# Kernel optimization log

Measured on AMD Instinct MI355X. Metric: run time of the kernel, lower is better.

Reference implementation:

```python
import jax, jax.numpy as jnp
import numpy as np

EMBED_DIM = 1280
NUM_HEADS = 20
HEAD_DIM = EMBED_DIM // NUM_HEADS


def setup_inputs() -> dict:
    key = jax.random.key(0)
    ks = jax.random.split(key, 9)
    s = 0.02
    return {
        "hidden_states": jax.random.normal(ks[0], (4, 1500, EMBED_DIM), dtype=jnp.float32),
        "q_w": jax.random.normal(ks[1], (EMBED_DIM, EMBED_DIM), dtype=jnp.float32) * s,
        "q_b": jax.random.normal(ks[2], (EMBED_DIM,), dtype=jnp.float32) * s,
        "k_w": jax.random.normal(ks[3], (EMBED_DIM, EMBED_DIM), dtype=jnp.float32) * s,
        "v_w": jax.random.normal(ks[4], (EMBED_DIM, EMBED_DIM), dtype=jnp.float32) * s,
        "v_b": jax.random.normal(ks[5], (EMBED_DIM,), dtype=jnp.float32) * s,
        "o_w": jax.random.normal(ks[6], (EMBED_DIM, EMBED_DIM), dtype=jnp.float32) * s,
        "o_b": jax.random.normal(ks[7], (EMBED_DIM,), dtype=jnp.float32) * s,
    }


def reference(hidden_states, q_w, q_b, k_w, v_w, v_b, o_w, o_b):
    B, T, E = hidden_states.shape
    H, D = NUM_HEADS, HEAD_DIM
    scaling = D ** (-0.5)
    # projections (torch Linear: x @ W^T + b)
    q = (hidden_states @ q_w.T + q_b) * scaling
    k = hidden_states @ k_w.T  # k_proj has bias=False
    v = hidden_states @ v_w.T + v_b
    # [B, H, T, D]
    q = q.reshape(B, T, H, D).transpose(0, 2, 1, 3)
    k = k.reshape(B, T, H, D).transpose(0, 2, 1, 3)
    v = v.reshape(B, T, H, D).transpose(0, 2, 1, 3)
    # NOTE: module divides by sqrt(head_dim) AGAIN inside the kernel (faithful)
    scores = jnp.einsum("bhqd,bhkd->bhqk", q, k) / jnp.sqrt(jnp.asarray(D, q.dtype))
    attn = jax.nn.softmax(scores, axis=-1)
    out = jnp.einsum("bhqk,bhkd->bhqd", attn, v)
    out = out.transpose(0, 2, 1, 3).reshape(B, T, E)
    return out @ o_w.T + o_b
```

## Files before the change

kernel.cpp:

```cpp
#include <hip/hip_runtime.h>

typedef __attribute__((ext_vector_type(4))) float f32x4;
typedef __attribute__((ext_vector_type(8))) __bf16 bf16x8;
typedef __attribute__((ext_vector_type(4))) __bf16 bf16x4;

#define DEV __device__ __forceinline__

DEV f32x4 mfma_bf16(bf16x8 a, bf16x8 b, f32x4 c) {
  return __builtin_amdgcn_mfma_f32_16x16x32_bf16(a, b, c, 0, 0, 0);
}

DEV void glds16(const void* gp, void* lp) {
  __builtin_amdgcn_global_load_lds((const __attribute__((address_space(1))) void*)gp,
                                   (__attribute__((address_space(3))) void*)lp, 16, 0, 0);
}

DEV float fast_exp2(float x) {
#if __has_builtin(__builtin_amdgcn_exp2f)
  return __builtin_amdgcn_exp2f(x);
#else
  float r;
  asm("v_exp_f32 %0, %1" : "=v"(r) : "v"(x));
  return r;
#endif
}

#define SB0() __builtin_amdgcn_sched_barrier(0)

__global__ __launch_bounds__(256) void cvt_all(const float* __restrict__ hs,
                                               const float* __restrict__ qw,
                                               const float* __restrict__ kw,
                                               const float* __restrict__ vw,
                                               const float* __restrict__ ow,
                                               __bf16* __restrict__ oX,
                                               __bf16* __restrict__ oQ,
                                               __bf16* __restrict__ oK,
                                               __bf16* __restrict__ oV,
                                               __bf16* __restrict__ oO) {
  const int blk = blockIdx.x;
  if (blk < 3840) {
    long long e = ((long long)blk * 256 + threadIdx.x) * 8;
    bf16x8 o = {};
    if (e < 7680000) {
      const f32x4* ip = (const f32x4*)(hs + e);
      f32x4 a = ip[0], b = ip[1];
#pragma unroll
      for (int j = 0; j < 4; ++j) { o[j] = (__bf16)a[j]; o[j + 4] = (__bf16)b[j]; }
    }
    *(bf16x8*)(oX + e) = o;
  } else {
    const int wb = blk - 3840;
    const int which = wb / 800;
    const int bb = wb - which * 800;
    const float* in = which == 0 ? qw : which == 1 ? kw : which == 2 ? vw : ow;
    __bf16* out = which == 0 ? oQ : which == 1 ? oK : which == 2 ? oV : oO;
    long long e = ((long long)bb * 256 + threadIdx.x) * 8;
    const f32x4* ip = (const f32x4*)(in + e);
    f32x4 x = ip[0], y = ip[1];
    bf16x8 o;
#pragma unroll
    for (int j = 0; j < 4; ++j) { o[j] = (__bf16)x[j]; o[j + 4] = (__bf16)y[j]; }
    *(bf16x8*)(out + e) = o;
  }
}

__global__ __launch_bounds__(512, 2) void gemm_qkv(const __bf16* __restrict__ A,
                                                   const __bf16* __restrict__ Bw,
                                                   const float* __restrict__ qbias,
                                                   const float* __restrict__ vbias,
                                                   __bf16* __restrict__ Qo,
                                                   __bf16* __restrict__ Ko,
                                                   __bf16* __restrict__ Vto,
                                                   float sq) {
  __shared__ __align__(16) __bf16 lds[3 * 24576];
  const int tid = threadIdx.x;
  const int lane = tid & 63, wave = tid >> 6;
  const int wrow = wave >> 2, wcol = wave & 3;
  const int r = lane & 15, g = lane >> 4;

  const int orig = blockIdx.x;
  const int xcd = orig & 7, ii = orig >> 3;
  const int m_idx = xcd * 6 + ii % 6;
  const int n_idx = ii / 6;
  const int m0 = m_idx * 128, n0 = n_idx * 256;

  const f32x4 fz = {0.f, 0.f, 0.f, 0.f};
  f32x4 acc[4][4];
#pragma unroll
  for (int mi = 0; mi < 4; ++mi)
#pragma unroll
    for (int ni = 0; ni < 4; ++ni) acc[mi][ni] = fz;

  const __bf16* srcA[2];
  const __bf16* srcB[4];
#pragma unroll
  for (int j = 0; j < 2; ++j) {
    const int slot = j * 512 + tid;
    const int row = slot >> 3, ch = slot & 7;
    srcA[j] = A + (size_t)(m0 + row) * 1280 + (ch ^ (row & 7)) * 8;
  }
#pragma unroll
  for (int j = 0; j < 4; ++j) {
    const int slot = j * 512 + tid;
    const int row = slot >> 3, ch = slot & 7;
    srcB[j] = Bw + (size_t)(n0 + row) * 1280 + (ch ^ (row & 7)) * 8;
  }
  const int wdst = wave * 512;

  auto stage_h0 = [&](int buf, int kt2) {
    const int k0 = kt2 * 64;
    glds16(srcA[0] + k0, &lds[buf * 24576 + wdst]);
    glds16(srcA[1] + k0, &lds[buf * 24576 + 4096 + wdst]);
    glds16(srcB[0] + k0, &lds[buf * 24576 + 8192 + wdst]);
  };
  auto stage_h1 = [&](int buf, int kt2) {
    const int k0 = kt2 * 64;
    glds16(srcB[1] + k0, &lds[buf * 24576 + 12288 + wdst]);
    glds16(srcB[2] + k0, &lds[buf * 24576 + 16384 + wdst]);
    glds16(srcB[3] + k0, &lds[buf * 24576 + 20480 + wdst]);
  };

  stage_h0(0, 0); stage_h1(0, 0);
  stage_h0(1, 1); stage_h1(1, 1);
  asm volatile("s_waitcnt vmcnt(6)" ::: "memory");
  SB0();
  __builtin_amdgcn_s_barrier();
  SB0();

  const int aoff = (wrow * 64 + r) * 64;
  const int boff = 8192 + (wcol * 64 + r) * 64;
  const int c0 = (g ^ (r & 7)) * 8;
  const int c1 = ((4 + g) ^ (r & 7)) * 8;

  int cur = 0;
  for (int kt = 0; kt < 20; ++kt) {
    int nxt2 = cur + 2; if (nxt2 >= 3) nxt2 -= 3;
    const __bf16* Lb = &lds[cur * 24576];
    const bool pf = (kt + 2 < 20);

    bf16x8 af[4], bfr[4];
#pragma unroll
    for (int mi = 0; mi < 4; ++mi) af[mi] = *(const bf16x8*)&Lb[aoff + mi * 1024 + c0];
#pragma unroll
    for (int ni = 0; ni < 4; ++ni) bfr[ni] = *(const bf16x8*)&Lb[boff + ni * 1024 + c0];
    if (pf) stage_h0(nxt2, kt + 2);
    asm volatile("s_waitcnt lgkmcnt(0)" ::: "memory");
    SB0();
    __builtin_amdgcn_s_setprio(1);
#pragma unroll
    for (int mi = 0; mi < 4; ++mi)
#pragma unroll
      for (int ni = 0; ni < 4; ++ni)
        acc[mi][ni] = mfma_bf16(af[mi], bfr[ni], acc[mi][ni]);
    __builtin_amdgcn_s_setprio(0);

    bf16x8 af1[4], bfr1[4];
#pragma unroll
    for (int mi = 0; mi < 4; ++mi) af1[mi] = *(const bf16x8*)&Lb[aoff + mi * 1024 + c1];
#pragma unroll
    for (int ni = 0; ni < 4; ++ni) bfr1[ni] = *(const bf16x8*)&Lb[boff + ni * 1024 + c1];
    if (pf) stage_h1(nxt2, kt + 2);
    asm volatile("s_waitcnt lgkmcnt(0)" ::: "memory");
    SB0();
    __builtin_amdgcn_s_setprio(1);
#pragma unroll
    for (int mi = 0; mi < 4; ++mi)
#pragma unroll
      for (int ni = 0; ni < 4; ++ni)
        acc[mi][ni] = mfma_bf16(af1[mi], bfr1[ni], acc[mi][ni]);
    __builtin_amdgcn_s_setprio(0);

    if (pf) asm volatile("s_waitcnt vmcnt(6)" ::: "memory");
    else    asm volatile("s_waitcnt vmcnt(0)" ::: "memory");
    SB0();
    __builtin_amdgcn_s_barrier();
    SB0();
    cur = cur + 1; if (cur >= 3) cur -= 3;
  }

  const int which = n_idx / 5;
  const int nb = n0 - which * 1280 + wcol * 64;
  const float scale = (which == 0) ? sq : 1.f;

#pragma unroll
  for (int ni = 0; ni < 4; ++ni) {
    const int col = nb + ni * 16 + r;
    const float bv = (which == 0) ? qbias[col] : (which == 2) ? vbias[col] : 0.f;
#pragma unroll
    for (int mi = 0; mi < 4; ++mi) {
      if (which == 2) {
        const int row0 = m0 + wrow * 64 + mi * 16 + g * 4;
        if (row0 < 6000) {
          const int bidx = row0 / 1500;
          const int t = row0 - bidx * 1500;
          union { __bf16 h[4]; unsigned long long u; } pk;
#pragma unroll
          for (int rr = 0; rr < 4; ++rr) pk.h[rr] = (__bf16)(acc[mi][ni][rr] + bv);
          *(unsigned long long*)&Vto[((size_t)(bidx * 1280 + col)) * 1536 + t] = pk.u;
        }
      } else {
        __bf16* dst = (which == 0) ? Qo : Ko;
#pragma unroll
        for (int rr = 0; rr < 4; ++rr) {
          const int row = m0 + wrow * 64 + mi * 16 + g * 4 + rr;
          dst[(size_t)row * 1280 + col] = (__bf16)((acc[mi][ni][rr] + bv) * scale);
        }
      }
    }
  }
}

__global__ __launch_bounds__(512, 2) void gemm_o(const __bf16* __restrict__ A,
                                                 const __bf16* __restrict__ Bw,
                                                 const float* __restrict__ bias,
                                                 float* __restrict__ out) {
  __shared__ __align__(16) __bf16 lds[3 * 24576];
  const int tid = threadIdx.x;
  const int lane = tid & 63, wave = tid >> 6;
  const int wrow = wave >> 2, wcol = wave & 3;
  const int r = lane & 15, g = lane >> 4;

  const int orig = blockIdx.x;
  const int xcd = orig & 7, ii = orig >> 3;
  const int m_idx = xcd * 6 + ii % 6;
  const int n_idx = ii / 6;
  const int m0 = m_idx * 128, n0 = n_idx * 256;

  const f32x4 fz = {0.f, 0.f, 0.f, 0.f};
  f32x4 acc[4][4];
#pragma unroll
  for (int mi = 0; mi < 4; ++mi)
#pragma unroll
    for (int ni = 0; ni < 4; ++ni) acc[mi][ni] = fz;

  const __bf16* srcA[2];
  const __bf16* srcB[4];
#pragma unroll
  for (int j = 0; j < 2; ++j) {
    const int slot = j * 512 + tid;
    const int row = slot >> 3, ch = slot & 7;
    srcA[j] = A + (size_t)(m0 + row) * 1280 + (ch ^ (row & 7)) * 8;
  }
#pragma unroll
  for (int j = 0; j < 4; ++j) {
    const int slot = j * 512 + tid;
    const int row = slot >> 3, ch = slot & 7;
    srcB[j] = Bw + (size_t)(n0 + row) * 1280 + (ch ^ (row & 7)) * 8;
  }
  const int wdst = wave * 512;

  auto stage_h0 = [&](int buf, int kt2) {
    const int k0 = kt2 * 64;
    glds16(srcA[0] + k0, &lds[buf * 24576 + wdst]);
    glds16(srcA[1] + k0, &lds[buf * 24576 + 4096 + wdst]);
    glds16(srcB[0] + k0, &lds[buf * 24576 + 8192 + wdst]);
  };
  auto stage_h1 = [&](int buf, int kt2) {
    const int k0 = kt2 * 64;
    glds16(srcB[1] + k0, &lds[buf * 24576 + 12288 + wdst]);
    glds16(srcB[2] + k0, &lds[buf * 24576 + 16384 + wdst]);
    glds16(srcB[3] + k0, &lds[buf * 24576 + 20480 + wdst]);
  };

  stage_h0(0, 0); stage_h1(0, 0);
  stage_h0(1, 1); stage_h1(1, 1);
  asm volatile("s_waitcnt vmcnt(6)" ::: "memory");
  SB0();
  __builtin_amdgcn_s_barrier();
  SB0();

  const int aoff = (wrow * 64 + r) * 64;
  const int boff = 8192 + (wcol * 64 + r) * 64;
  const int c0 = (g ^ (r & 7)) * 8;
  const int c1 = ((4 + g) ^ (r & 7)) * 8;

  int cur = 0;
  for (int kt = 0; kt < 20; ++kt) {
    int nxt2 = cur + 2; if (nxt2 >= 3) nxt2 -= 3;
    const __bf16* Lb = &lds[cur * 24576];
    const bool pf = (kt + 2 < 20);

    bf16x8 af[4], bfr[4];
#pragma unroll
    for (int mi = 0; mi < 4; ++mi) af[mi] = *(const bf16x8*)&Lb[aoff + mi * 1024 + c0];
#pragma unroll
    for (int ni = 0; ni < 4; ++ni) bfr[ni] = *(const bf16x8*)&Lb[boff + ni * 1024 + c0];
    if (pf) stage_h0(nxt2, kt + 2);
    asm volatile("s_waitcnt lgkmcnt(0)" ::: "memory");
    SB0();
    __builtin_amdgcn_s_setprio(1);
#pragma unroll
    for (int mi = 0; mi < 4; ++mi)
#pragma unroll
      for (int ni = 0; ni < 4; ++ni)
        acc[mi][ni] = mfma_bf16(af[mi], bfr[ni], acc[mi][ni]);
    __builtin_amdgcn_s_setprio(0);

    bf16x8 af1[4], bfr1[4];
#pragma unroll
    for (int mi = 0; mi < 4; ++mi) af1[mi] = *(const bf16x8*)&Lb[aoff + mi * 1024 + c1];
#pragma unroll
    for (int ni = 0; ni < 4; ++ni) bfr1[ni] = *(const bf16x8*)&Lb[boff + ni * 1024 + c1];
    if (pf) stage_h1(nxt2, kt + 2);
    asm volatile("s_waitcnt lgkmcnt(0)" ::: "memory");
    SB0();
    __builtin_amdgcn_s_setprio(1);
#pragma unroll
    for (int mi = 0; mi < 4; ++mi)
#pragma unroll
      for (int ni = 0; ni < 4; ++ni)
        acc[mi][ni] = mfma_bf16(af1[mi], bfr1[ni], acc[mi][ni]);
    __builtin_amdgcn_s_setprio(0);

    if (pf) asm volatile("s_waitcnt vmcnt(6)" ::: "memory");
    else    asm volatile("s_waitcnt vmcnt(0)" ::: "memory");
    SB0();
    __builtin_amdgcn_s_barrier();
    SB0();
    cur = cur + 1; if (cur >= 3) cur -= 3;
  }

#pragma unroll
  for (int ni = 0; ni < 4; ++ni) {
    const int col = n0 + wcol * 64 + ni * 16 + r;
    const float bv = bias[col];
#pragma unroll
    for (int mi = 0; mi < 4; ++mi) {
#pragma unroll
      for (int rr = 0; rr < 4; ++rr) {
        const int row = m0 + wrow * 64 + mi * 16 + g * 4 + rr;
        if (row < 6000) out[(size_t)row * 1280 + col] = acc[mi][ni][rr] + bv;
      }
    }
  }
}

__global__ __launch_bounds__(256) void flash_attn(const __bf16* __restrict__ Qg,
                                                  const __bf16* __restrict__ Kg,
                                                  const __bf16* __restrict__ Vt,
                                                  __bf16* __restrict__ Og) {
  constexpr int TQ = 1500, NKT = 24;
  __shared__ __align__(16) __bf16 lds[16384];

  const int tid = threadIdx.x;
  const int lane = tid & 63, w = tid >> 6;
  const int r = lane & 15, g = lane >> 4;

  const int orig = blockIdx.x;
  const int work = (orig & 7) * 120 + (orig >> 3);
  const int bh = work / 12, qb = work - bh * 12;
  const int b = bh / 20, h = bh - b * 20;
  const int q0 = qb * 128;
  const size_t base = (size_t)b * (TQ * 1280) + h * 64;
  const __bf16* Vt_bh = Vt + (size_t)(b * 1280 + h * 64) * 1536;

  const int k_src_col = 8 * ((lane & 7) ^ (lane >> 3));
  const int k_row_loc = w * 8 + (lane >> 3);
  const int v_d_loc = 8 * w + (lane >> 3);
  const int v_chunk = 8 * ((lane & 7) ^ (lane >> 3));

  bf16x8 qf[2][2];
#pragma unroll
  for (int qs = 0; qs < 2; ++qs) {
    int t = q0 + w * 32 + qs * 16 + r;
    t = t < TQ ? t : TQ - 1;
    const __bf16* qp = Qg + base + (size_t)t * 1280;
#pragma unroll
    for (int dk = 0; dk < 2; ++dk) qf[qs][dk] = *(const bf16x8*)(qp + dk * 32 + g * 8);
  }

  const f32x4 fz = {0.f, 0.f, 0.f, 0.f};
  f32x4 o_acc[2][4];
#pragma unroll
  for (int qs = 0; qs < 2; ++qs)
#pragma unroll
    for (int ni = 0; ni < 4; ++ni) o_acc[qs][ni] = fz;
  float l_run[2] = {0.f, 0.f};

  auto stage = [&](int buf, int kt2) {
    const int kb = kt2 * 64;
#pragma unroll
    for (int i = 0; i < 2; ++i) {
      int row = kb + i * 32 + k_row_loc;
      row = row < TQ ? row : TQ - 1;
      glds16(Kg + base + (size_t)row * 1280 + k_src_col,
             &lds[buf * 8192 + i * 2048 + w * 512]);
    }
#pragma unroll
    for (int i = 0; i < 2; ++i) {
      glds16(Vt_bh + (size_t)(32 * i + v_d_loc) * 1536 + kb + v_chunk,
             &lds[buf * 8192 + 4096 + i * 2048 + w * 512]);
    }
  };

  stage(0, 0);
  for (int kt = 0; kt < NKT; ++kt) {
    const int cur = kt & 1;
    if (kt + 1 < NKT) {
      stage(cur ^ 1, kt + 1);
      asm volatile("s_waitcnt vmcnt(4)" ::: "memory");
    } else {
      asm volatile("s_waitcnt vmcnt(0)" ::: "memory");
    }
    SB0();
    __builtin_amdgcn_s_barrier();
    SB0();

    const __bf16* Kb = &lds[cur * 8192];

    f32x4 s[2][4];
#pragma unroll
    for (int qs = 0; qs < 2; ++qs)
#pragma unroll
      for (int nt = 0; nt < 4; ++nt) s[qs][nt] = fz;
#pragma unroll
    for (int dk = 0; dk < 2; ++dk) {
      bf16x8 kf[4];
#pragma unroll
      for (int nt = 0; nt < 4; ++nt) {
        const int row = nt * 16 + r;
        const int sc = (dk * 32 + g * 8) ^ ((r & 7) << 3);
        kf[nt] = *(const bf16x8*)&Kb[row * 64 + sc];
      }
#pragma unroll
      for (int qs = 0; qs < 2; ++qs)
#pragma unroll
        for (int nt = 0; nt < 4; ++nt) s[qs][nt] = mfma_bf16(kf[nt], qf[qs][dk], s[qs][nt]);
    }

    if (kt == NKT - 1) {
#pragma unroll
      for (int nt = 0; nt < 4; ++nt)
#pragma unroll
        for (int rr = 0; rr < 4; ++rr) {
          const int key = kt * 64 + nt * 16 + g * 4 + rr;
          if (key >= TQ) { s[0][nt][rr] = -1.0e30f; s[1][nt][rr] = -1.0e30f; }
        }
    }

#pragma unroll
    for (int qs = 0; qs < 2; ++qs) {
      float ssum = 0.f;
#pragma unroll
      for (int nt = 0; nt < 4; ++nt)
#pragma unroll
        for (int rr = 0; rr < 4; ++rr) {
          const float p = fast_exp2(s[qs][nt][rr]);
          s[qs][nt][rr] = p;
          ssum += p;
        }
      l_run[qs] += ssum;
    }

    const __bf16* Vbuf = &lds[cur * 8192 + 4096];
    const int swz = (r & 7) << 3;
#pragma unroll
    for (int ks = 0; ks < 2; ++ks) {
      bf16x8 pa[2];
#pragma unroll
      for (int qs = 0; qs < 2; ++qs) {
        bf16x8 t;
#pragma unroll
        for (int j = 0; j < 4; ++j) {
          t[j] = (__bf16)s[qs][2 * ks][j];
          t[4 + j] = (__bf16)s[qs][2 * ks + 1][j];
        }
        pa[qs] = t;
      }
      const int o1 = (32 * ks + 4 * g) ^ swz;
      const int o2 = (32 * ks + 16 + 4 * g) ^ swz;
#pragma unroll
      for (int ni = 0; ni < 4; ++ni) {
        const int dbase = (16 * ni + r) * 64;
        union { bf16x4 hh[2]; bf16x8 v; } u;
        u.hh[0] = *(const bf16x4*)&Vbuf[dbase + o1];
        u.hh[1] = *(const bf16x4*)&Vbuf[dbase + o2];
#pragma unroll
        for (int qs = 0; qs < 2; ++qs) o_acc[qs][ni] = mfma_bf16(u.v, pa[qs], o_acc[qs][ni]);
      }
    }

    asm volatile("s_waitcnt lgkmcnt(0)" ::: "memory");
    SB0();
    __builtin_amdgcn_s_barrier();
    SB0();
  }

  float inv[2];
#pragma unroll
  for (int qs = 0; qs < 2; ++qs) {
    float l = l_run[qs];
    l += __shfl_xor(l, 16);
    l += __shfl_xor(l, 32);
    inv[qs] = 1.0f / l;
  }

  __bf16* Ob = &lds[w * 2304];
#pragma unroll
  for (int qs = 0; qs < 2; ++qs) {
#pragma unroll
    for (int ni = 0; ni < 4; ++ni)
#pragma unroll
      for (int rr = 0; rr < 4; ++rr)
        Ob[(qs * 16 + r) * 72 + ni * 16 + g * 4 + rr] = (__bf16)(o_acc[qs][ni][rr] * inv[qs]);
  }
  __syncthreads();
  const int qg = q0 + w * 32 + (lane >> 1);
  if (qg < TQ) {
#pragma unroll
    for (int v = 0; v < 4; ++v) {
      const int c = (lane & 1) * 32 + v * 8;
      bf16x8 val = *(const bf16x8*)&lds[w * 2304 + (lane >> 1) * 72 + c];
      *(bf16x8*)&Og[base + (size_t)qg * 1280 + c] = val;
    }
  }
}

extern "C" void kernel_launch(void* const* d_in, const int* in_sizes, int n_in,
                              void* d_out, int out_size, void* d_ws, size_t ws_size,
                              hipStream_t stream) {
  const float* hs = (const float*)d_in[0];
  const float* qw = (const float*)d_in[1];
  const float* qb = (const float*)d_in[2];
  const float* kw = (const float*)d_in[3];
  const float* vw = (const float*)d_in[4];
  const float* vb = (const float*)d_in[5];
  const float* ow = (const float*)d_in[6];
  const float* ob = (const float*)d_in[7];

  const long long MP = 6144LL * 1280;
  const long long WE = 1280LL * 1280;
  __bf16* Xb = (__bf16*)d_ws;
  __bf16* Wq = Xb + MP;
  __bf16* Wk = Wq + WE;
  __bf16* Wv = Wk + WE;
  __bf16* Wo = Wv + WE;
  __bf16* Qb = Wo + WE;
  __bf16* Kb = Qb + MP;
  __bf16* Vtb = Kb + MP;
  __bf16* Ab = Xb;

  cvt_all<<<7040, 256, 0, stream>>>(hs, qw, kw, vw, ow, Xb, Wq, Wk, Wv, Wo);

  const float SQ = 1.4426950408889634f / 64.f;
  gemm_qkv<<<720, 512, 0, stream>>>(Xb, Wq, qb, vb, Qb, Kb, Vtb, SQ);

  flash_attn<<<960, 256, 0, stream>>>(Qb, Kb, Vtb, Ab);

  gemm_o<<<240, 512, 0, stream>>>(Ab, Wo, ob, (float*)d_out);
}
```

Baseline: 175.7 us.

## Load K and V fragments directly from global memory into registers in flash attention

```diff
diff --git a/kernel.cpp b/kernel.cpp
--- a/kernel.cpp
+++ b/kernel.cpp
@@ -340,7 +340,7 @@
                                                   const __bf16* __restrict__ Vt,
                                                   __bf16* __restrict__ Og) {
   constexpr int TQ = 1500, NKT = 24;
-  __shared__ __align__(16) __bf16 lds[16384];
+  __shared__ __align__(16) __bf16 lds[4 * 2304];
 
   const int tid = threadIdx.x;
   const int lane = tid & 63, w = tid >> 6;
@@ -354,11 +354,6 @@
   const size_t base = (size_t)b * (TQ * 1280) + h * 64;
   const __bf16* Vt_bh = Vt + (size_t)(b * 1280 + h * 64) * 1536;
 
-  const int k_src_col = 8 * ((lane & 7) ^ (lane >> 3));
-  const int k_row_loc = w * 8 + (lane >> 3);
-  const int v_d_loc = 8 * w + (lane >> 3);
-  const int v_chunk = 8 * ((lane & 7) ^ (lane >> 3));
-
   bf16x8 qf[2][2];
 #pragma unroll
   for (int qs = 0; qs < 2; ++qs) {
@@ -377,36 +372,33 @@
     for (int ni = 0; ni < 4; ++ni) o_acc[qs][ni] = fz;
   float l_run[2] = {0.f, 0.f};
 
-  auto stage = [&](int buf, int kt2) {
-    const int kb = kt2 * 64;
-#pragma unroll
-    for (int i = 0; i < 2; ++i) {
-      int row = kb + i * 32 + k_row_loc;
+  const __bf16* vrow[4];
+#pragma unroll
+  for (int ni = 0; ni < 4; ++ni) vrow[ni] = Vt_bh + (size_t)(16 * ni + r) * 1536 + 4 * g;
+
+  for (int kt = 0; kt < NKT; ++kt) {
+    const int kb = kt * 64;
+
+    bf16x8 kf[2][4];
+#pragma unroll
+    for (int nt = 0; nt < 4; ++nt) {
+      int row = kb + nt * 16 + r;
       row = row < TQ ? row : TQ - 1;
-      glds16(Kg + base + (size_t)row * 1280 + k_src_col,
-             &lds[buf * 8192 + i * 2048 + w * 512]);
-    }
-#pragma unroll
-    for (int i = 0; i < 2; ++i) {
-      glds16(Vt_bh + (size_t)(32 * i + v_d_loc) * 1536 + kb + v_chunk,
-             &lds[buf * 8192 + 4096 + i * 2048 + w * 512]);
-    }
-  };
-
-  stage(0, 0);
-  for (int kt = 0; kt < NKT; ++kt) {
-    const int cur = kt & 1;
-    if (kt + 1 < NKT) {
-      stage(cur ^ 1, kt + 1);
-      asm volatile("s_waitcnt vmcnt(4)" ::: "memory");
-    } else {
-      asm volatile("s_waitcnt vmcnt(0)" ::: "memory");
-    }
-    SB0();
-    __builtin_amdgcn_s_barrier();
-    SB0();
-
-    const __bf16* Kb = &lds[cur * 8192];
+      const __bf16* kp = Kg + base + (size_t)row * 1280 + g * 8;
+      kf[0][nt] = *(const bf16x8*)kp;
+      kf[1][nt] = *(const bf16x8*)(kp + 32);
+    }
+
+    bf16x4 vfl[2][4][2];
+#pragma unroll
+    for (int ni = 0; ni < 4; ++ni) {
+      const __bf16* vp = vrow[ni] + kb;
+#pragma unroll
+      for (int ks = 0; ks < 2; ++ks) {
+        vfl[ks][ni][0] = *(const bf16x4*)(vp + 32 * ks);
+        vfl[ks][ni][1] = *(const bf16x4*)(vp + 32 * ks + 16);
+      }
+    }
 
     f32x4 s[2][4];
 #pragma unroll
@@ -414,26 +406,19 @@
 #pragma unroll
       for (int nt = 0; nt < 4; ++nt) s[qs][nt] = fz;
 #pragma unroll
-    for (int dk = 0; dk < 2; ++dk) {
-      bf16x8 kf[4];
-#pragma unroll
-      for (int nt = 0; nt < 4; ++nt) {
-        const int row = nt * 16 + r;
-        const int sc = (dk * 32 + g * 8) ^ ((r & 7) << 3);
-        kf[nt] = *(const bf16x8*)&Kb[row * 64 + sc];
-      }
+    for (int dk = 0; dk < 2; ++dk)
 #pragma unroll
       for (int qs = 0; qs < 2; ++qs)
 #pragma unroll
-        for (int nt = 0; nt < 4; ++nt) s[qs][nt] = mfma_bf16(kf[nt], qf[qs][dk], s[qs][nt]);
-    }
+        for (int nt = 0; nt < 4; ++nt)
+          s[qs][nt] = mfma_bf16(kf[dk][nt], qf[qs][dk], s[qs][nt]);
 
     if (kt == NKT - 1) {
 #pragma unroll
       for (int nt = 0; nt < 4; ++nt)
 #pragma unroll
         for (int rr = 0; rr < 4; ++rr) {
-          const int key = kt * 64 + nt * 16 + g * 4 + rr;
+          const int key = kb + nt * 16 + g * 4 + rr;
           if (key >= TQ) { s[0][nt][rr] = -1.0e30f; s[1][nt][rr] = -1.0e30f; }
         }
     }
@@ -452,8 +437,6 @@
       l_run[qs] += ssum;
     }
 
-    const __bf16* Vbuf = &lds[cur * 8192 + 4096];
-    const int swz = (r & 7) << 3;
 #pragma unroll
     for (int ks = 0; ks < 2; ++ks) {
       bf16x8 pa[2];
@@ -467,23 +450,15 @@
         }
         pa[qs] = t;
       }
-      const int o1 = (32 * ks + 4 * g) ^ swz;
-      const int o2 = (32 * ks + 16 + 4 * g) ^ swz;
 #pragma unroll
       for (int ni = 0; ni < 4; ++ni) {
-        const int dbase = (16 * ni + r) * 64;
         union { bf16x4 hh[2]; bf16x8 v; } u;
-        u.hh[0] = *(const bf16x4*)&Vbuf[dbase + o1];
-        u.hh[1] = *(const bf16x4*)&Vbuf[dbase + o2];
+        u.hh[0] = vfl[ks][ni][0];
+        u.hh[1] = vfl[ks][ni][1];
 #pragma unroll
         for (int qs = 0; qs < 2; ++qs) o_acc[qs][ni] = mfma_bf16(u.v, pa[qs], o_acc[qs][ni]);
       }
     }
-
-    asm volatile("s_waitcnt lgkmcnt(0)" ::: "memory");
-    SB0();
-    __builtin_amdgcn_s_barrier();
-    SB0();
   }
 
   float inv[2];
```

Result: slower. 419.6 us (+138.8%).

## Split flash attention across eight waves of sixteen queries each

Applied to the files above, without the earlier changes.

```diff
diff --git a/kernel.cpp b/kernel.cpp
--- a/kernel.cpp
+++ b/kernel.cpp
@@ -335,7 +335,7 @@
   }
 }
 
-__global__ __launch_bounds__(256) void flash_attn(const __bf16* __restrict__ Qg,
+__global__ __launch_bounds__(512) void flash_attn(const __bf16* __restrict__ Qg,
                                                   const __bf16* __restrict__ Kg,
                                                   const __bf16* __restrict__ Vt,
                                                   __bf16* __restrict__ Og) {
@@ -354,65 +354,45 @@
   const size_t base = (size_t)b * (TQ * 1280) + h * 64;
   const __bf16* Vt_bh = Vt + (size_t)(b * 1280 + h * 64) * 1536;
 
-  const int k_src_col = 8 * ((lane & 7) ^ (lane >> 3));
   const int k_row_loc = w * 8 + (lane >> 3);
-  const int v_d_loc = 8 * w + (lane >> 3);
-  const int v_chunk = 8 * ((lane & 7) ^ (lane >> 3));
-
-  bf16x8 qf[2][2];
-#pragma unroll
-  for (int qs = 0; qs < 2; ++qs) {
-    int t = q0 + w * 32 + qs * 16 + r;
+  const int kv_chunk = 8 * ((lane & 7) ^ (lane >> 3));
+
+  bf16x8 qf[2];
+  {
+    int t = q0 + w * 16 + r;
     t = t < TQ ? t : TQ - 1;
     const __bf16* qp = Qg + base + (size_t)t * 1280;
 #pragma unroll
-    for (int dk = 0; dk < 2; ++dk) qf[qs][dk] = *(const bf16x8*)(qp + dk * 32 + g * 8);
+    for (int dk = 0; dk < 2; ++dk) qf[dk] = *(const bf16x8*)(qp + dk * 32 + g * 8);
   }
 
   const f32x4 fz = {0.f, 0.f, 0.f, 0.f};
-  f32x4 o_acc[2][4];
-#pragma unroll
-  for (int qs = 0; qs < 2; ++qs)
-#pragma unroll
-    for (int ni = 0; ni < 4; ++ni) o_acc[qs][ni] = fz;
-  float l_run[2] = {0.f, 0.f};
+  f32x4 o_acc[4];
+#pragma unroll
+  for (int ni = 0; ni < 4; ++ni) o_acc[ni] = fz;
+  float l_run = 0.f;
 
   auto stage = [&](int buf, int kt2) {
     const int kb = kt2 * 64;
-#pragma unroll
-    for (int i = 0; i < 2; ++i) {
-      int row = kb + i * 32 + k_row_loc;
-      row = row < TQ ? row : TQ - 1;
-      glds16(Kg + base + (size_t)row * 1280 + k_src_col,
-             &lds[buf * 8192 + i * 2048 + w * 512]);
-    }
-#pragma unroll
-    for (int i = 0; i < 2; ++i) {
-      glds16(Vt_bh + (size_t)(32 * i + v_d_loc) * 1536 + kb + v_chunk,
-             &lds[buf * 8192 + 4096 + i * 2048 + w * 512]);
-    }
+    int row = kb + k_row_loc;
+    row = row < TQ ? row : TQ - 1;
+    glds16(Kg + base + (size_t)row * 1280 + kv_chunk,
+           &lds[buf * 8192 + w * 512]);
+    glds16(Vt_bh + (size_t)k_row_loc * 1536 + kb + kv_chunk,
+           &lds[buf * 8192 + 4096 + w * 512]);
   };
 
   stage(0, 0);
+  __syncthreads();
   for (int kt = 0; kt < NKT; ++kt) {
     const int cur = kt & 1;
-    if (kt + 1 < NKT) {
-      stage(cur ^ 1, kt + 1);
-      asm volatile("s_waitcnt vmcnt(4)" ::: "memory");
-    } else {
-      asm volatile("s_waitcnt vmcnt(0)" ::: "memory");
-    }
-    SB0();
-    __builtin_amdgcn_s_barrier();
-    SB0();
+    if (kt + 1 < NKT) stage(cur ^ 1, kt + 1);
 
     const __bf16* Kb = &lds[cur * 8192];
 
-    f32x4 s[2][4];
-#pragma unroll
-    for (int qs = 0; qs < 2; ++qs)
-#pragma unroll
-      for (int nt = 0; nt < 4; ++nt) s[qs][nt] = fz;
+    f32x4 s[4];
+#pragma unroll
+    for (int nt = 0; nt < 4; ++nt) s[nt] = fz;
 #pragma unroll
     for (int dk = 0; dk < 2; ++dk) {
       bf16x8 kf[4];
@@ -423,9 +403,7 @@
         kf[nt] = *(const bf16x8*)&Kb[row * 64 + sc];
       }
 #pragma unroll
-      for (int qs = 0; qs < 2; ++qs)
-#pragma unroll
-        for (int nt = 0; nt < 4; ++nt) s[qs][nt] = mfma_bf16(kf[nt], qf[qs][dk], s[qs][nt]);
+      for (int nt = 0; nt < 4; ++nt) s[nt] = mfma_bf16(kf[nt], qf[dk], s[nt]);
     }
 
     if (kt == NKT - 1) {
@@ -434,38 +412,32 @@
 #pragma unroll
         for (int rr = 0; rr < 4; ++rr) {
           const int key = kt * 64 + nt * 16 + g * 4 + rr;
-          if (key >= TQ) { s[0][nt][rr] = -1.0e30f; s[1][nt][rr] = -1.0e30f; }
+          if (key >= TQ) s[nt][rr] = -1.0e30f;
         }
     }
 
-#pragma unroll
-    for (int qs = 0; qs < 2; ++qs) {
+    {
       float ssum = 0.f;
 #pragma unroll
       for (int nt = 0; nt < 4; ++nt)
 #pragma unroll
         for (int rr = 0; rr < 4; ++rr) {
-          const float p = fast_exp2(s[qs][nt][rr]);
-          s[qs][nt][rr] = p;
+          const float p = fast_exp2(s[nt][rr]);
+          s[nt][rr] = p;
           ssum += p;
         }
-      l_run[qs] += ssum;
+      l_run += ssum;
     }
 
     const __bf16* Vbuf = &lds[cur * 8192 + 4096];
     const int swz = (r & 7) << 3;
 #pragma unroll
     for (int ks = 0; ks < 2; ++ks) {
-      bf16x8 pa[2];
-#pragma unroll
-      for (int qs = 0; qs < 2; ++qs) {
-        bf16x8 t;
-#pragma unroll
-        for (int j = 0; j < 4; ++j) {
-          t[j] = (__bf16)s[qs][2 * ks][j];
-          t[4 + j] = (__bf16)s[qs][2 * ks + 1][j];
-        }
-        pa[qs] = t;
+      bf16x8 pa;
+#pragma unroll
+      for (int j = 0; j < 4; ++j) {
+        pa[j] = (__bf16)s[2 * ks][j];
+        pa[4 + j] = (__bf16)s[2 * ks + 1][j];
       }
       const int o1 = (32 * ks + 4 * g) ^ swz;
       const int o2 = (32 * ks + 16 + 4 * g) ^ swz;
@@ -475,42 +447,31 @@
         union { bf16x4 hh[2]; bf16x8 v; } u;
         u.hh[0] = *(const bf16x4*)&Vbuf[dbase + o1];
         u.hh[1] = *(const bf16x4*)&Vbuf[dbase + o2];
-#pragma unroll
-        for (int qs = 0; qs < 2; ++qs) o_acc[qs][ni] = mfma_bf16(u.v, pa[qs], o_acc[qs][ni]);
+        o_acc[ni] = mfma_bf16(u.v, pa, o_acc[ni]);
       }
     }
 
-    asm volatile("s_waitcnt lgkmcnt(0)" ::: "memory");
-    SB0();
-    __builtin_amdgcn_s_barrier();
-    SB0();
-  }
-
-  float inv[2];
-#pragma unroll
-  for (int qs = 0; qs < 2; ++qs) {
-    float l = l_run[qs];
-    l += __shfl_xor(l, 16);
-    l += __shfl_xor(l, 32);
-    inv[qs] = 1.0f / l;
-  }
-
-  __bf16* Ob = &lds[w * 2304];
-#pragma unroll
-  for (int qs = 0; qs < 2; ++qs) {
-#pragma unroll
-    for (int ni = 0; ni < 4; ++ni)
-#pragma unroll
-      for (int rr = 0; rr < 4; ++rr)
-        Ob[(qs * 16 + r) * 72 + ni * 16 + g * 4 + rr] = (__bf16)(o_acc[qs][ni][rr] * inv[qs]);
-  }
+    __syncthreads();
+  }
+
+  float l = l_run;
+  l += __shfl_xor(l, 16);
+  l += __shfl_xor(l, 32);
+  const float inv = 1.0f / l;
+
+  __bf16* Ob = &lds[w * 1152];
+#pragma unroll
+  for (int ni = 0; ni < 4; ++ni)
+#pragma unroll
+    for (int rr = 0; rr < 4; ++rr)
+      Ob[r * 72 + ni * 16 + g * 4 + rr] = (__bf16)(o_acc[ni][rr] * inv);
   __syncthreads();
-  const int qg = q0 + w * 32 + (lane >> 1);
+  const int qg = q0 + w * 16 + (lane >> 2);
   if (qg < TQ) {
 #pragma unroll
-    for (int v = 0; v < 4; ++v) {
-      const int c = (lane & 1) * 32 + v * 8;
-      bf16x8 val = *(const bf16x8*)&lds[w * 2304 + (lane >> 1) * 72 + c];
+    for (int v = 0; v < 2; ++v) {
+      const int c = (lane & 3) * 16 + v * 8;
+      bf16x8 val = *(const bf16x8*)&lds[w * 1152 + (lane >> 2) * 72 + c];
       *(bf16x8*)&Og[base + (size_t)qg * 1280 + c] = val;
     }
   }
@@ -545,7 +506,7 @@
   const float SQ = 1.4426950408889634f / 64.f;
   gemm_qkv<<<720, 512, 0, stream>>>(Xb, Wq, qb, vb, Qb, Kb, Vtb, SQ);
 
-  flash_attn<<<960, 256, 0, stream>>>(Qb, Kb, Vtb, Ab);
+  flash_attn<<<960, 512, 0, stream>>>(Qb, Kb, Vtb, Ab);
 
   gemm_o<<<240, 512, 0, stream>>>(Ab, Wo, ob, (float*)d_out);
 }
```

After: 175.4 us. Within noise of the previous version (-0.2%).

## Compute softmax row sums with MFMA, merge barriers, prioritize MFMA waves

Applied to the files above, without the earlier changes.

```diff
diff --git a/kernel.cpp b/kernel.cpp
--- a/kernel.cpp
+++ b/kernel.cpp
@@ -369,13 +369,18 @@
     for (int dk = 0; dk < 2; ++dk) qf[qs][dk] = *(const bf16x8*)(qp + dk * 32 + g * 8);
   }
 
+  bf16x8 ones;
+#pragma unroll
+  for (int j = 0; j < 8; ++j) ones[j] = (__bf16)1.0f;
+
   const f32x4 fz = {0.f, 0.f, 0.f, 0.f};
-  f32x4 o_acc[2][4];
-#pragma unroll
-  for (int qs = 0; qs < 2; ++qs)
+  f32x4 o_acc[2][4], o_sum[2];
+#pragma unroll
+  for (int qs = 0; qs < 2; ++qs) {
+    o_sum[qs] = fz;
 #pragma unroll
     for (int ni = 0; ni < 4; ++ni) o_acc[qs][ni] = fz;
-  float l_run[2] = {0.f, 0.f};
+  }
 
   auto stage = [&](int buf, int kt2) {
     const int kb = kt2 * 64;
@@ -394,17 +399,10 @@
   };
 
   stage(0, 0);
+  __syncthreads();
   for (int kt = 0; kt < NKT; ++kt) {
     const int cur = kt & 1;
-    if (kt + 1 < NKT) {
-      stage(cur ^ 1, kt + 1);
-      asm volatile("s_waitcnt vmcnt(4)" ::: "memory");
-    } else {
-      asm volatile("s_waitcnt vmcnt(0)" ::: "memory");
-    }
-    SB0();
-    __builtin_amdgcn_s_barrier();
-    SB0();
+    if (kt + 1 < NKT) stage(cur ^ 1, kt + 1);
 
     const __bf16* Kb = &lds[cur * 8192];
 
@@ -422,10 +420,12 @@
         const int sc = (dk * 32 + g * 8) ^ ((r & 7) << 3);
         kf[nt] = *(const bf16x8*)&Kb[row * 64 + sc];
       }
+      __builtin_amdgcn_s_setprio(1);
 #pragma unroll
       for (int qs = 0; qs < 2; ++qs)
 #pragma unroll
         for (int nt = 0; nt < 4; ++nt) s[qs][nt] = mfma_bf16(kf[nt], qf[qs][dk], s[qs][nt]);
+      __builtin_amdgcn_s_setprio(0);
     }
 
     if (kt == NKT - 1) {
@@ -439,18 +439,12 @@
     }
 
 #pragma unroll
-    for (int qs = 0; qs < 2; ++qs) {
-      float ssum = 0.f;
+    for (int qs = 0; qs < 2; ++qs)
 #pragma unroll
       for (int nt = 0; nt < 4; ++nt)
 #pragma unroll
-        for (int rr = 0; rr < 4; ++rr) {
-          const float p = fast_exp2(s[qs][nt][rr]);
-          s[qs][nt][rr] = p;
-          ssum += p;
-        }
-      l_run[qs] += ssum;
-    }
+        for (int rr = 0; rr < 4; ++rr)
+          s[qs][nt][rr] = fast_exp2(s[qs][nt][rr]);
 
     const __bf16* Vbuf = &lds[cur * 8192 + 4096];
     const int swz = (r & 7) << 3;
@@ -469,6 +463,9 @@
       }
       const int o1 = (32 * ks + 4 * g) ^ swz;
       const int o2 = (32 * ks + 16 + 4 * g) ^ swz;
+      __builtin_amdgcn_s_setprio(1);
+#pragma unroll
+      for (int qs = 0; qs < 2; ++qs) o_sum[qs] = mfma_bf16(ones, pa[qs], o_sum[qs]);
 #pragma unroll
       for (int ni = 0; ni < 4; ++ni) {
         const int dbase = (16 * ni + r) * 64;
@@ -478,22 +475,15 @@
 #pragma unroll
         for (int qs = 0; qs < 2; ++qs) o_acc[qs][ni] = mfma_bf16(u.v, pa[qs], o_acc[qs][ni]);
       }
-    }
-
-    asm volatile("s_waitcnt lgkmcnt(0)" ::: "memory");
-    SB0();
-    __builtin_amdgcn_s_barrier();
-    SB0();
+      __builtin_amdgcn_s_setprio(0);
+    }
+
+    __syncthreads();
   }
 
   float inv[2];
 #pragma unroll
-  for (int qs = 0; qs < 2; ++qs) {
-    float l = l_run[qs];
-    l += __shfl_xor(l, 16);
-    l += __shfl_xor(l, 32);
-    inv[qs] = 1.0f / l;
-  }
+  for (int qs = 0; qs < 2; ++qs) inv[qs] = 1.0f / o_sum[qs][0];
 
   __bf16* Ob = &lds[w * 2304];
 #pragma unroll
```

Result: no change. 173.3 us (-1.3%).
